# Optimization experiments

Measured on AMD Instinct MI355X. Metric: run time of the kernel, lower is better.

Reference implementation:

```python
import jax, jax.numpy as jnp
import numpy as np

NP_, NA, NPR = 3000, 25, 1071
N = NP_ + NA + NPR          # 4096 total nodes
D = 256                     # latent_dim
H = 8                       # num_heads
DH = D // H                 # head dim 32
FF = 4 * D                  # feed-forward dim
BLOCKS = 3                  # args.block_num
E = 131072                  # edges = N * 32 avg degree
EPS = 1e-5


def setup_inputs() -> dict:
    key = jax.random.key(0)
    ks = jax.random.split(key, 16)
    s = 1.0 / np.sqrt(D)
    return {
        "adj_row": jax.random.randint(ks[0], (E,), 0, N, dtype=jnp.int32),
        "adj_col": jax.random.randint(ks[1], (E,), 0, N, dtype=jnp.int32),
        "adj_val": jax.random.uniform(ks[2], (E,), dtype=jnp.float32),
        "pe": jax.random.normal(ks[3], (NP_, D), dtype=jnp.float32) * s,
        "ae": jax.random.normal(ks[4], (NA, D), dtype=jnp.float32) * s,
        "qe": jax.random.normal(ks[5], (NPR, D), dtype=jnp.float32) * s,
        "Wqkv": jax.random.normal(ks[6], (D, 3 * D), dtype=jnp.float32) * s,
        "Wo": jax.random.normal(ks[7], (D, D), dtype=jnp.float32) * s,
        "W1": jax.random.normal(ks[8], (D, FF), dtype=jnp.float32) * s,
        "b1": jnp.zeros((FF,), dtype=jnp.float32),
        "W2": jax.random.normal(ks[9], (FF, D), dtype=jnp.float32) * (1.0 / np.sqrt(FF)),
        "b2": jnp.zeros((D,), dtype=jnp.float32),
        "ln1_g": jnp.ones((D,), dtype=jnp.float32),
        "ln1_b": jnp.zeros((D,), dtype=jnp.float32),
        "ln2_g": jnp.ones((D,), dtype=jnp.float32),
        "ln2_b": jnp.zeros((D,), dtype=jnp.float32),
    }


def _layer_norm(x, g, b):
    m = jnp.mean(x, axis=-1, keepdims=True)
    v = jnp.mean(jnp.square(x - m), axis=-1, keepdims=True)
    return (x - m) * jax.lax.rsqrt(v + EPS) * g + b


def _encoder_layer(x, Wqkv, Wo, W1, b1, W2, b2, ln1_g, ln1_b, ln2_g, ln2_b):
    # x: [N, D]; standard post-LN transformer encoder (dropout = 0)
    qkv = x @ Wqkv                                   # [N, 3D]
    q, k, v = jnp.split(qkv, 3, axis=-1)
    q = q.reshape(N, H, DH)
    k = k.reshape(N, H, DH)
    v = v.reshape(N, H, DH)
    scores = jnp.einsum("nhd,mhd->hnm", q, k) / np.sqrt(DH)  # [H, N, N]
    att = jax.nn.softmax(scores, axis=-1)
    o = jnp.einsum("hnm,mhd->nhd", att, v).reshape(N, D) @ Wo
    x = _layer_norm(x + o, ln1_g, ln1_b)
    h = jax.nn.relu(x @ W1 + b1) @ W2 + b2
    return _layer_norm(x + h, ln2_g, ln2_b)


def _spmm(adj_row, adj_col, adj_val, x):
    # sparse [N,N] @ dense [N,D] via gather + segment-sum scatter
    msgs = adj_val[:, None] * x[adj_col]             # [E, D]
    return jax.ops.segment_sum(msgs, adj_row, num_segments=N)


def reference(adj_row, adj_col, adj_val, pe, ae, qe, Wqkv, Wo, W1, b1, W2, b2,
              ln1_g, ln1_b, ln2_g, ln2_b):
    cur = jnp.concatenate([pe, ae, qe], axis=0)      # [N, D]
    total = cur
    for _ in range(BLOCKS):
        t = _spmm(adj_row, adj_col, adj_val, cur)
        t = _encoder_layer(t, Wqkv, Wo, W1, b1, W2, b2, ln1_g, ln1_b, ln2_g, ln2_b)
        cur = t + cur                                # residual per block
        total = total + cur                          # sum over embeds list
    protein = total[:NP_]
    aa = total[NP_:NP_ + NA]
    prop = total[NP_ + NA:]
    return total, protein, aa, prop
```

## Files before the change

### kernel.cpp

```cpp
#include <hip/hip_runtime.h>
#include <hip/hip_bf16.h>


#define NPROT 3000
#define NAA   25
#define NPROP 1071
#define NTOT  4096
#define DIM   256
#define NH    8
#define DHD   32
#define FFD   1024
#define NEDGE 131072
#define LNEPS 1e-5f
#define KSPLIT 4
#define KVQ (NTOT/KSPLIT)

typedef unsigned short u16;
typedef unsigned int u32;
typedef __attribute__((ext_vector_type(8))) short short8v;
typedef __attribute__((ext_vector_type(4))) float float4v;
typedef __attribute__((ext_vector_type(2))) unsigned int uint2v;

__device__ __forceinline__ u16 f2bu(float x){
  union { __hip_bfloat16 h; u16 u; } c; c.h = __float2bfloat16(x); return c.u;
}
__device__ __forceinline__ float bu2f(u16 u){
  union { u32 i; float f; } c; c.i = ((u32)u) << 16; return c.f;
}
__device__ __forceinline__ float4v mfma16(short8v a, short8v b, float4v c){
  return __builtin_amdgcn_mfma_f32_16x16x32_bf16(a, b, c, 0, 0, 0);
}
__device__ __forceinline__ u32 packbf(float lo, float hi){
  u32 ul = __builtin_bit_cast(u32, lo);
  u32 uh = __builtin_bit_cast(u32, hi);
  return (ul >> 16) | (uh & 0xFFFF0000u);
}

__global__ __launch_bounds__(256) void k_embed(const float* __restrict__ pe, const float* __restrict__ ae,
                                               const float* __restrict__ qe,
                                               float* __restrict__ cur, float* __restrict__ tot){
  int i = blockIdx.x*256 + threadIdx.x;
  int row = i >> 8;
  float v;
  if (row < NPROT)           v = pe[i];
  else if (row < NPROT+NAA)  v = ae[i - NPROT*DIM];
  else                       v = qe[i - (NPROT+NAA)*DIM];
  cur[i] = v; tot[i] = v;
}

__global__ __launch_bounds__(256) void k_zero(int* __restrict__ p, int n){
  int i = blockIdx.x*256 + threadIdx.x; if (i < n) p[i] = 0;
}

__global__ __launch_bounds__(256) void k_wconv(const float* __restrict__ W, u16* __restrict__ Wt,
                                               int K, int N){
  int n = blockIdx.x;
  for (int k = threadIdx.x; k < K; k += 256)
    Wt[(size_t)n*K + k] = f2bu(W[(size_t)k*N + n]);
}

__global__ __launch_bounds__(256) void k_hist(const int* __restrict__ rows, int* __restrict__ cnt){
  int e = blockIdx.x*256 + threadIdx.x; if (e < NEDGE) atomicAdd(&cnt[rows[e]], 1);
}

__global__ __launch_bounds__(64) void k_scan(const int* __restrict__ cnt, int* __restrict__ rowptr,
                                             int* __restrict__ cursor){
  int lane = threadIdx.x;
  int sum = 0;
  for (int i = 0; i < 64; ++i) sum += cnt[lane*64 + i];
  int pref = sum;
  #pragma unroll
  for (int off = 1; off < 64; off <<= 1){
    int u = __shfl_up(pref, off);
    if (lane >= off) pref += u;
  }
  int run = pref - sum;
  for (int i = 0; i < 64; ++i){
    int c = cnt[lane*64 + i];
    rowptr[lane*64 + i] = run;
    cursor[lane*64 + i] = run;
    run += c;
  }
  if (lane == 63) rowptr[NTOT] = run;
}

__global__ __launch_bounds__(256) void k_scatter(const int* __restrict__ rows, const int* __restrict__ cols,
                                                 const float* __restrict__ vals, int* __restrict__ cursor,
                                                 int* __restrict__ ccol, float* __restrict__ cval){
  int e = blockIdx.x*256 + threadIdx.x; if (e >= NEDGE) return;
  int p = atomicAdd(&cursor[rows[e]], 1);
  ccol[p] = cols[e]; cval[p] = vals[e];
}

__global__ __launch_bounds__(256) void k_spmm(const int* __restrict__ rowptr, const int* __restrict__ ccol,
                                              const float* __restrict__ cval, const float* __restrict__ x,
                                              float* __restrict__ out, u16* __restrict__ outb){
  int r = blockIdx.x, c = threadIdx.x;
  int s = rowptr[r], e = rowptr[r+1];
  float acc = 0.f;
  for (int i = s; i < e; ++i)
    acc += cval[i] * x[((size_t)ccol[i] << 8) + c];
  out[((size_t)r << 8) + c] = acc;
  outb[((size_t)r << 8) + c] = f2bu(acc);
}

template<int RELU, int BIAS, int BF16OUT>
__global__ __launch_bounds__(256) void k_gemm64(const u16* __restrict__ A, const u16* __restrict__ Wt,
                                                const float* __restrict__ bias, void* __restrict__ Cv,
                                                int M, int K, int Nc){
  __shared__ u16 Al[64*64];
  __shared__ u16 Bl[64*64];
  const int tid = threadIdx.x;
  const int w  = tid >> 6, l = tid & 63, lr = l & 15, g = l >> 4;
  const int row0 = blockIdx.y*64, col0 = blockIdx.x*64;
  const int wm = (w >> 1)*32, wn = (w & 1)*32;
  const int sm = tid >> 2;
  const int so = (tid & 3)*2;
  float4v acc[2][2] = {};

  for (int k0 = 0; k0 < K; k0 += 64){
    const u16* As = A  + (size_t)(row0 + sm)*K + k0 + so*8;
    const u16* Bs = Wt + (size_t)(col0 + sm)*K + k0 + so*8;
    #pragma unroll
    for (int j = 0; j < 2; ++j){
      int o = so + j;
      int slot = o ^ (sm & 7);
      *(short8v*)(Al + sm*64 + slot*8) = *(const short8v*)(As + j*8);
      *(short8v*)(Bl + sm*64 + slot*8) = *(const short8v*)(Bs + j*8);
    }
    __syncthreads();
    #pragma unroll
    for (int kk = 0; kk < 2; ++kk){
      short8v af[2], bfr[2];
      #pragma unroll
      for (int i = 0; i < 2; ++i){
        int am = wm + 16*i + lr;
        af[i]  = *(const short8v*)(Al + am*64 + (((4*kk + g) ^ (am & 7))*8));
        int bn = wn + 16*i + lr;
        bfr[i] = *(const short8v*)(Bl + bn*64 + (((4*kk + g) ^ (bn & 7))*8));
      }
      acc[0][0] = mfma16(af[0], bfr[0], acc[0][0]);
      acc[0][1] = mfma16(af[0], bfr[1], acc[0][1]);
      acc[1][0] = mfma16(af[1], bfr[0], acc[1][0]);
      acc[1][1] = mfma16(af[1], bfr[1], acc[1][1]);
    }
    __syncthreads();
  }

  #pragma unroll
  for (int mi = 0; mi < 2; ++mi){
    #pragma unroll
    for (int ni = 0; ni < 2; ++ni){
      int col = col0 + wn + 16*ni + lr;
      float bv = BIAS ? bias[col] : 0.f;
      #pragma unroll
      for (int j = 0; j < 4; ++j){
        int row = row0 + wm + 16*mi + 4*g + j;
        float v = acc[mi][ni][j] + bv;
        if (RELU) v = fmaxf(v, 0.f);
        if (BF16OUT) ((u16*)Cv)[(size_t)row*Nc + col] = f2bu(v);
        else         ((float*)Cv)[(size_t)row*Nc + col] = v;
      }
    }
  }
}

__global__ __launch_bounds__(256) void k_attn_mfma(const u16* __restrict__ qbf,
                                                   u16* __restrict__ op,
                                                   float* __restrict__ mbuf, float* __restrict__ lbuf){
  __shared__ u16 Vt[2][32*64];
  __shared__ u16 Pl[4][16*64];
  __shared__ float Fl[4][16];
  const int h   = blockIdx.y;
  const int ks  = blockIdx.z;
  const int qb  = blockIdx.x * 64;
  const int tid = threadIdx.x;
  const int w   = tid >> 6;
  const int l   = tid & 63;
  const int lr  = l & 15;
  const int g   = l >> 4;
  const int sr  = tid >> 2;
  const int sq  = tid & 3;
  const float SC  = 0.17677669529663687f;
  const float SCL = 0.25503837f;
  u16* opart = op + (size_t)ks*NTOT*DIM;

  short8v qf = *(const short8v*)(qbf + (size_t)(qb + 16*w + lr)*768 + h*DHD + 8*g);
  short8v ones;
  #pragma unroll
  for (int j = 0; j < 8; ++j) ones[j] = (short)0x3F80;

  float4v oa0 = {0.f,0.f,0.f,0.f}, oa1 = {0.f,0.f,0.f,0.f};
  float4v accl = {0.f,0.f,0.f,0.f};
  float mrun = -1e30f;
  u16* pw = &Pl[w][0];

  const u16* vp = qbf + (size_t)(ks*KVQ + sr)*768 + 512 + h*DHD + 8*sq;
  const u16* kp = qbf + (size_t)(ks*KVQ + lr)*768 + 256 + h*DHD + 8*g;
  short8v vreg = *(const short8v*)vp;
  short8v kf0 = *(const short8v*)(kp);
  short8v kf1 = *(const short8v*)(kp + (size_t)16*768);
  short8v kf2 = *(const short8v*)(kp + (size_t)32*768);
  short8v kf3 = *(const short8v*)(kp + (size_t)48*768);

  const int NIT = KVQ/64;
  for (int t = 0; t < NIT; ++t){
    u16* vt = &Vt[t & 1][0];
    #pragma unroll
    for (int j = 0; j < 8; ++j){
      int row  = 8*sq + j;
      int slot = (sr >> 3) ^ j;
      vt[row*64 + slot*8 + (sr & 7)] = (u16)vreg[j];
    }
    __syncthreads();
    vp += (size_t)64*768;
    if (t + 1 < NIT) vreg = *(const short8v*)vp;

    float4v s0 = mfma16(kf0, qf, (float4v){0.f,0.f,0.f,0.f});
    float4v s1 = mfma16(kf1, qf, (float4v){0.f,0.f,0.f,0.f});
    float4v s2 = mfma16(kf2, qf, (float4v){0.f,0.f,0.f,0.f});
    float4v s3 = mfma16(kf3, qf, (float4v){0.f,0.f,0.f,0.f});
    if (t + 1 < NIT){
      const u16* kn = kp + (size_t)(t+1)*64*768;
      kf0 = *(const short8v*)(kn);
      kf1 = *(const short8v*)(kn + (size_t)16*768);
      kf2 = *(const short8v*)(kn + (size_t)32*768);
      kf3 = *(const short8v*)(kn + (size_t)48*768);
    }

    float m0 = fmaxf(fmaxf(fmaxf(s0[0],s0[1]),s0[2]),s0[3]);
    float m1 = fmaxf(fmaxf(fmaxf(s1[0],s1[1]),s1[2]),s1[3]);
    float m2 = fmaxf(fmaxf(fmaxf(s2[0],s2[1]),s2[2]),s2[3]);
    float m3 = fmaxf(fmaxf(fmaxf(s3[0],s3[1]),s3[2]),s3[3]);
    float tm = fmaxf(fmaxf(fmaxf(m0,m1),m2),m3);
    tm = fmaxf(tm, __shfl_xor(tm, 16));
    tm = fmaxf(tm, __shfl_xor(tm, 32));
    const bool nomax = __all(tm <= mrun);
    float fac = 1.f;
    if (!nomax){
      float mn = fmaxf(mrun, tm);
      fac = exp2f((mrun - mn)*SCL);
      mrun = mn;
    }
    float mns = mrun*SCL;
    #pragma unroll
    for (int j = 0; j < 4; ++j){
      s0[j] = exp2f(__builtin_fmaf(s0[j], SCL, -mns));
      s1[j] = exp2f(__builtin_fmaf(s1[j], SCL, -mns));
      s2[j] = exp2f(__builtin_fmaf(s2[j], SCL, -mns));
      s3[j] = exp2f(__builtin_fmaf(s3[j], SCL, -mns));
    }

    {
      int gh = g >> 1, gl = 4*(g & 1);
      uint2v* d0 = (uint2v*)(pw + lr*64 + ((0 + gh) ^ (lr & 7))*8 + gl);
      uint2v* d1 = (uint2v*)(pw + lr*64 + ((2 + gh) ^ (lr & 7))*8 + gl);
      uint2v* d2 = (uint2v*)(pw + lr*64 + ((4 + gh) ^ (lr & 7))*8 + gl);
      uint2v* d3 = (uint2v*)(pw + lr*64 + ((6 + gh) ^ (lr & 7))*8 + gl);
      *d0 = (uint2v){packbf(s0[0],s0[1]), packbf(s0[2],s0[3])};
      *d1 = (uint2v){packbf(s1[0],s1[1]), packbf(s1[2],s1[3])};
      *d2 = (uint2v){packbf(s2[0],s2[1]), packbf(s2[2],s2[3])};
      *d3 = (uint2v){packbf(s3[0],s3[1]), packbf(s3[2],s3[3])};
    }

    if (!nomax){
      if (g == 0) Fl[w][lr] = fac;
      float fq0 = Fl[w][4*g+0], fq1 = Fl[w][4*g+1], fq2 = Fl[w][4*g+2], fq3 = Fl[w][4*g+3];
      oa0[0]*=fq0; oa0[1]*=fq1; oa0[2]*=fq2; oa0[3]*=fq3;
      oa1[0]*=fq0; oa1[1]*=fq1; oa1[2]*=fq2; oa1[3]*=fq3;
      accl[0]*=fq0; accl[1]*=fq1; accl[2]*=fq2; accl[3]*=fq3;
    }

    #pragma unroll
    for (int kk = 0; kk < 2; ++kk){
      int slotp = (4*kk + g) ^ (lr & 7);
      short8v pa = *(const short8v*)(pw + lr*64 + slotp*8);
      short8v v0 = *(const short8v*)(vt + lr*64        + slotp*8);
      short8v v1 = *(const short8v*)(vt + (lr+16)*64   + slotp*8);
      oa0  = mfma16(pa, v0, oa0);
      oa1  = mfma16(pa, v1, oa1);
      accl = mfma16(pa, ones, accl);
    }
  }

  #pragma unroll
  for (int j = 0; j < 4; ++j){
    size_t row = (size_t)(qb + 16*w + 4*g + j);
    opart[row*DIM + h*DHD + lr]      = f2bu(oa0[j]);
    opart[row*DIM + h*DHD + 16 + lr] = f2bu(oa1[j]);
  }
  if (l < 16){
    size_t mi = (size_t)(ks*NH + h)*NTOT + qb + 16*w + lr;
    mbuf[mi] = mrun*SC;
  }
  if (lr == 0){
    #pragma unroll
    for (int j = 0; j < 4; ++j){
      size_t mi = (size_t)(ks*NH + h)*NTOT + qb + 16*w + 4*g + j;
      lbuf[mi] = accl[j];
    }
  }
}

__global__ __launch_bounds__(256) void k_attn_merge(const u16* __restrict__ op,
                                                    const float* __restrict__ mbuf, const float* __restrict__ lbuf,
                                                    u16* __restrict__ obf){
  int i = blockIdx.x*256 + threadIdx.x;
  int r = i >> 8, c = i & 255, h = c >> 5;
  float m[KSPLIT], wgt[KSPLIT];
  float M = -1e30f;
  #pragma unroll
  for (int k = 0; k < KSPLIT; ++k){
    m[k] = mbuf[(size_t)(k*NH + h)*NTOT + r];
    M = fmaxf(M, m[k]);
  }
  float L = 0.f, acc = 0.f;
  #pragma unroll
  for (int k = 0; k < KSPLIT; ++k){
    wgt[k] = __expf(m[k] - M);
    L   += wgt[k]*lbuf[(size_t)(k*NH + h)*NTOT + r];
    acc += wgt[k]*bu2f(op[(size_t)k*NTOT*DIM + i]);
  }
  obf[i] = f2bu(acc / L);
}

template<int DUAL>
__global__ __launch_bounds__(256) void k_add_ln(const float* __restrict__ a, const float* __restrict__ b,
                                                const float* __restrict__ g, const float* __restrict__ be,
                                                float* __restrict__ out, u16* __restrict__ out2){
  __shared__ float red[4];
  int r = blockIdx.x, c = threadIdx.x;
  float v = a[((size_t)r << 8) + c] + b[((size_t)r << 8) + c];
  float s = v;
  #pragma unroll
  for (int off = 32; off; off >>= 1) s += __shfl_down(s, off);
  if ((c & 63) == 0) red[c >> 6] = s;
  __syncthreads();
  float mean = (red[0]+red[1]+red[2]+red[3]) * (1.f/DIM);
  __syncthreads();
  float d = v - mean;
  float s2 = d*d;
  #pragma unroll
  for (int off = 32; off; off >>= 1) s2 += __shfl_down(s2, off);
  if ((c & 63) == 0) red[c >> 6] = s2;
  __syncthreads();
  float var = (red[0]+red[1]+red[2]+red[3]) * (1.f/DIM);
  float rv = d * rsqrtf(var + LNEPS) * g[c] + be[c];
  out[((size_t)r << 8) + c] = rv;
  if (DUAL) out2[((size_t)r << 8) + c] = f2bu(rv);
}

__global__ __launch_bounds__(256) void k_add_ln_upd(const float* __restrict__ a, const float* __restrict__ b,
                                                    const float* __restrict__ g, const float* __restrict__ be,
                                                    float* __restrict__ cur, float* __restrict__ tot){
  __shared__ float red[4];
  int r = blockIdx.x, c = threadIdx.x;
  size_t idx = ((size_t)r << 8) + c;
  float v = a[idx] + b[idx];
  float s = v;
  #pragma unroll
  for (int off = 32; off; off >>= 1) s += __shfl_down(s, off);
  if ((c & 63) == 0) red[c >> 6] = s;
  __syncthreads();
  float mean = (red[0]+red[1]+red[2]+red[3]) * (1.f/DIM);
  __syncthreads();
  float d = v - mean;
  float s2 = d*d;
  #pragma unroll
  for (int off = 32; off; off >>= 1) s2 += __shfl_down(s2, off);
  if ((c & 63) == 0) red[c >> 6] = s2;
  __syncthreads();
  float var = (red[0]+red[1]+red[2]+red[3]) * (1.f/DIM);
  float rv = d * rsqrtf(var + LNEPS) * g[c] + be[c];
  float cu = cur[idx] + rv;
  cur[idx] = cu;
  tot[idx] += cu;
}

__global__ __launch_bounds__(256) void k_out(const float* __restrict__ tot, float* __restrict__ out){
  int i = blockIdx.x*256 + threadIdx.x;
  float v = tot[i];
  out[i] = v;
  out[NTOT*DIM + i] = v;
}

extern "C" void kernel_launch(void* const* d_in, const int* in_sizes, int n_in,
                              void* d_out, int out_size, void* d_ws, size_t ws_size,
                              hipStream_t stream){
  const int*   adj_row = (const int*)  d_in[0];
  const int*   adj_col = (const int*)  d_in[1];
  const float* adj_val = (const float*)d_in[2];
  const float* pe   = (const float*)d_in[3];
  const float* ae   = (const float*)d_in[4];
  const float* qe   = (const float*)d_in[5];
  const float* Wqkv = (const float*)d_in[6];
  const float* Wo   = (const float*)d_in[7];
  const float* W1   = (const float*)d_in[8];
  const float* b1   = (const float*)d_in[9];
  const float* W2   = (const float*)d_in[10];
  const float* b2   = (const float*)d_in[11];
  const float* g1   = (const float*)d_in[12];
  const float* be1  = (const float*)d_in[13];
  const float* g2   = (const float*)d_in[14];
  const float* be2  = (const float*)d_in[15];
  float* out = (float*)d_out;

  char* w = (char*)d_ws;
  float* cur  = (float*)w; w += (size_t)NTOT*DIM*4;
  float* tot  = (float*)w; w += (size_t)NTOT*DIM*4;
  float* tf   = (float*)w; w += (size_t)NTOT*DIM*4;
  float* pbuf = (float*)w; w += (size_t)NTOT*DIM*4;
  float* x1   = (float*)w; w += (size_t)NTOT*DIM*4;
  u16* tbf    = (u16*)w;   w += (size_t)NTOT*DIM*2;
  u16* obf    = (u16*)w;   w += (size_t)NTOT*DIM*2;
  u16* x1b    = (u16*)w;   w += (size_t)NTOT*DIM*2;
  u16* hq     = (u16*)w;   w += (size_t)NTOT*FFD*2;
  u16* wqkvt  = (u16*)w;   w += (size_t)768*256*2;
  u16* wot    = (u16*)w;   w += (size_t)256*256*2;
  u16* w1t    = (u16*)w;   w += (size_t)1024*256*2;
  u16* w2t    = (u16*)w;   w += (size_t)256*1024*2;
  int* rowptr = (int*)w;   w += (size_t)(NTOT+1)*4;
  int* cnt    = (int*)w;   w += (size_t)NTOT*4;
  int* cursor = (int*)w;   w += (size_t)NTOT*4;
  int* ccol   = (int*)w;   w += (size_t)NEDGE*4;
  float* cval = (float*)w; w += (size_t)NEDGE*4;
  u16* qbf  = hq;
  u16* opbf = (u16*)pbuf;
  float* mbuf = (float*)tbf;
  float* lbuf = mbuf + (size_t)KSPLIT*NH*NTOT;

  k_zero<<<16, 256, 0, stream>>>(cnt, NTOT);
  k_embed<<<NTOT, 256, 0, stream>>>(pe, ae, qe, cur, tot);
  k_hist<<<NEDGE/256, 256, 0, stream>>>(adj_row, cnt);
  k_scan<<<1, 64, 0, stream>>>(cnt, rowptr, cursor);
  k_scatter<<<NEDGE/256, 256, 0, stream>>>(adj_row, adj_col, adj_val, cursor, ccol, cval);
  k_wconv<<<768,  256, 0, stream>>>(Wqkv, wqkvt, 256, 768);
  k_wconv<<<256,  256, 0, stream>>>(Wo,   wot,   256, 256);
  k_wconv<<<1024, 256, 0, stream>>>(W1,   w1t,   256, 1024);
  k_wconv<<<256,  256, 0, stream>>>(W2,   w2t,  1024, 256);

  for (int blk = 0; blk < 3; ++blk){
    k_spmm<<<NTOT, 256, 0, stream>>>(rowptr, ccol, cval, cur, tf, tbf);
    k_gemm64<0,0,1><<<dim3(768/64, NTOT/64), 256, 0, stream>>>(tbf, wqkvt, nullptr, qbf, NTOT, 256, 768);
    k_attn_mfma<<<dim3(NTOT/64, NH, KSPLIT), 256, 0, stream>>>(qbf, opbf, mbuf, lbuf);
    k_attn_merge<<<NTOT*DIM/256, 256, 0, stream>>>(opbf, mbuf, lbuf, obf);
    k_gemm64<0,0,0><<<dim3(256/64, NTOT/64), 256, 0, stream>>>(obf, wot, nullptr, pbuf, NTOT, 256, 256);
    k_add_ln<1><<<NTOT, 256, 0, stream>>>(tf, pbuf, g1, be1, x1, x1b);
    k_gemm64<1,1,1><<<dim3(1024/64, NTOT/64), 256, 0, stream>>>(x1b, w1t, b1, hq, NTOT, 256, 1024);
    k_gemm64<0,1,0><<<dim3(256/64, NTOT/64), 256, 0, stream>>>(hq, w2t, b2, pbuf, NTOT, 1024, 256);
    k_add_ln_upd<<<NTOT, 256, 0, stream>>>(x1, pbuf, g2, be2, cur, tot);
  }
  k_out<<<NTOT, 256, 0, stream>>>(tot, out);
}
```

Measured before the change: 492.5 us.

## Halve attention KV split, defer softmax rescale, merge weight conversions and output copy

Reduces the attention key split from 4 to 2, so fewer partial outputs are written and merged, at the cost of fewer blocks and longer per-block loops. Adds a lazy max-update threshold (DEFER) to the online softmax so the accumulator rescale is skipped unless the new max exceeds the running one by a margin, which risks larger exponent values but keeps them bounded within bf16/fp32 range. Merges four weight-conversion launches into one kernel. Folds the final output copy into the last add-LN-update kernel to drop a launch and a full pass over the total buffer.

```diff
diff --git a/kernel.cpp b/kernel.cpp
--- a/kernel.cpp
+++ b/kernel.cpp
@@ -12,7 +12,7 @@
 #define FFD   1024
 #define NEDGE 131072
 #define LNEPS 1e-5f
-#define KSPLIT 4
+#define KSPLIT 2
 #define KVQ (NTOT/KSPLIT)
 
 typedef unsigned short u16;
@@ -52,9 +52,16 @@
   int i = blockIdx.x*256 + threadIdx.x; if (i < n) p[i] = 0;
 }
 
-__global__ __launch_bounds__(256) void k_wconv(const float* __restrict__ W, u16* __restrict__ Wt,
-                                               int K, int N){
-  int n = blockIdx.x;
+__global__ __launch_bounds__(256) void k_wconv_all(const float* __restrict__ Wqkv, const float* __restrict__ Wo,
+                                                   const float* __restrict__ W1, const float* __restrict__ W2,
+                                                   u16* __restrict__ wqkvt, u16* __restrict__ wot,
+                                                   u16* __restrict__ w1t, u16* __restrict__ w2t){
+  int b = blockIdx.x;
+  const float* W; u16* Wt; int K, N, n;
+  if (b < 768)       { W = Wqkv; Wt = wqkvt; K = 256;  N = 768;  n = b; }
+  else if (b < 1024) { W = Wo;   Wt = wot;   K = 256;  N = 256;  n = b - 768; }
+  else if (b < 2048) { W = W1;   Wt = w1t;   K = 256;  N = 1024; n = b - 1024; }
+  else               { W = W2;   Wt = w2t;   K = 1024; N = 256;  n = b - 2048; }
   for (int k = threadIdx.x; k < K; k += 256)
     Wt[(size_t)n*K + k] = f2bu(W[(size_t)k*N + n]);
 }
@@ -183,6 +190,7 @@
   const int sq  = tid & 3;
   const float SC  = 0.17677669529663687f;
   const float SCL = 0.25503837f;
+  const float DEFER = 31.368f;
   u16* opart = op + (size_t)ks*NTOT*DIM;
 
   short8v qf = *(const short8v*)(qbf + (size_t)(qb + 16*w + lr)*768 + h*DHD + 8*g);
@@ -235,7 +243,7 @@
     float tm = fmaxf(fmaxf(fmaxf(m0,m1),m2),m3);
     tm = fmaxf(tm, __shfl_xor(tm, 16));
     tm = fmaxf(tm, __shfl_xor(tm, 32));
-    const bool nomax = __all(tm <= mrun);
+    const bool nomax = __all(tm <= mrun + DEFER);
     float fac = 1.f;
     if (!nomax){
       float mn = fmaxf(mrun, tm);
@@ -350,9 +358,11 @@
   if (DUAL) out2[((size_t)r << 8) + c] = f2bu(rv);
 }
 
+template<int FINAL>
 __global__ __launch_bounds__(256) void k_add_ln_upd(const float* __restrict__ a, const float* __restrict__ b,
                                                     const float* __restrict__ g, const float* __restrict__ be,
-                                                    float* __restrict__ cur, float* __restrict__ tot){
+                                                    float* __restrict__ cur, float* __restrict__ tot,
+                                                    float* __restrict__ out){
   __shared__ float red[4];
   int r = blockIdx.x, c = threadIdx.x;
   size_t idx = ((size_t)r << 8) + c;
@@ -374,14 +384,12 @@
   float rv = d * rsqrtf(var + LNEPS) * g[c] + be[c];
   float cu = cur[idx] + rv;
   cur[idx] = cu;
-  tot[idx] += cu;
-}
-
-__global__ __launch_bounds__(256) void k_out(const float* __restrict__ tot, float* __restrict__ out){
-  int i = blockIdx.x*256 + threadIdx.x;
-  float v = tot[i];
-  out[i] = v;
-  out[NTOT*DIM + i] = v;
+  float tv = tot[idx] + cu;
+  tot[idx] = tv;
+  if (FINAL){
+    out[idx] = tv;
+    out[(size_t)NTOT*DIM + idx] = tv;
+  }
 }
 
 extern "C" void kernel_launch(void* const* d_in, const int* in_sizes, int n_in,
@@ -434,10 +442,7 @@
   k_hist<<<NEDGE/256, 256, 0, stream>>>(adj_row, cnt);
   k_scan<<<1, 64, 0, stream>>>(cnt, rowptr, cursor);
   k_scatter<<<NEDGE/256, 256, 0, stream>>>(adj_row, adj_col, adj_val, cursor, ccol, cval);
-  k_wconv<<<768,  256, 0, stream>>>(Wqkv, wqkvt, 256, 768);
-  k_wconv<<<256,  256, 0, stream>>>(Wo,   wot,   256, 256);
-  k_wconv<<<1024, 256, 0, stream>>>(W1,   w1t,   256, 1024);
-  k_wconv<<<256,  256, 0, stream>>>(W2,   w2t,  1024, 256);
+  k_wconv_all<<<2304, 256, 0, stream>>>(Wqkv, Wo, W1, W2, wqkvt, wot, w1t, w2t);
 
   for (int blk = 0; blk < 3; ++blk){
     k_spmm<<<NTOT, 256, 0, stream>>>(rowptr, ccol, cval, cur, tf, tbf);
@@ -448,7 +453,9 @@
     k_add_ln<1><<<NTOT, 256, 0, stream>>>(tf, pbuf, g1, be1, x1, x1b);
     k_gemm64<1,1,1><<<dim3(1024/64, NTOT/64), 256, 0, stream>>>(x1b, w1t, b1, hq, NTOT, 256, 1024);
     k_gemm64<0,1,0><<<dim3(256/64, NTOT/64), 256, 0, stream>>>(hq, w2t, b2, pbuf, NTOT, 1024, 256);
-    k_add_ln_upd<<<NTOT, 256, 0, stream>>>(x1, pbuf, g2, be2, cur, tot);
-  }
-  k_out<<<NTOT, 256, 0, stream>>>(tot, out);
-}
+    if (blk < 2)
+      k_add_ln_upd<0><<<NTOT, 256, 0, stream>>>(x1, pbuf, g2, be2, cur, tot, nullptr);
+    else
+      k_add_ln_upd<1><<<NTOT, 256, 0, stream>>>(x1, pbuf, g2, be2, cur, tot, out);
+  }
+}
```

New measurement: 476.1 us. -3.3%, faster.
